# Optimization experiments

Measured on AMD Instinct MI355X. Metric: run time of the kernel, lower is better.

Reference implementation:

```python
import jax, jax.numpy as jnp
import numpy as np

N_NODES = 50000
N_EDGES = 800000
IN_FEAT = 256
OUT_FEAT = 256
NUM_RELS = 64
NUM_BASES = 8


def setup_inputs() -> dict:
    key = jax.random.key(0)
    ks = jax.random.split(key, 9)
    x = jax.random.normal(ks[0], (N_NODES, IN_FEAT), dtype=jnp.float32)
    src = jax.random.randint(ks[1], (N_EDGES,), 0, N_NODES, dtype=jnp.int32)
    dst = jax.random.randint(ks[2], (N_EDGES,), 0, N_NODES, dtype=jnp.int32)
    etypes = jax.random.randint(ks[3], (N_EDGES,), 0, NUM_RELS, dtype=jnp.int32)
    norm = jax.random.uniform(ks[4], (N_EDGES, 1), dtype=jnp.float32)
    # glorot-style params
    s_w = (6.0 / (IN_FEAT + OUT_FEAT)) ** 0.5
    weight = jax.random.uniform(ks[5], (NUM_BASES, IN_FEAT, OUT_FEAT), jnp.float32, -s_w, s_w)
    s_c = (6.0 / (NUM_RELS + NUM_BASES)) ** 0.5
    w_comp = jax.random.uniform(ks[6], (NUM_RELS, NUM_BASES), jnp.float32, -s_c, s_c)
    h_bias = jnp.zeros((OUT_FEAT,), jnp.float32)
    loop_weight = jax.random.uniform(ks[7], (IN_FEAT, OUT_FEAT), jnp.float32, -s_w, s_w)
    return {"x": x, "src": src, "dst": dst, "etypes": etypes, "norm": norm,
            "weight": weight, "w_comp": w_comp, "h_bias": h_bias,
            "loop_weight": loop_weight}


def reference(x, src, dst, etypes, norm, weight, w_comp, h_bias, loop_weight):
    # Basis regularizer with num_bases < num_rels:
    #   W_r = sum_b w_comp[r, b] * V_b
    # Per-edge message: msg_e = (x[src_e] @ W_{etype_e}) * norm_e,
    # aggregated by sum onto destination nodes. Since the map is linear,
    # we aggregate per basis first, then apply V_b (8 dense GEMMs).
    n_nodes = x.shape[0]
    coef = w_comp[etypes]                      # [E, B] per-edge basis coeffs
    xs = x[src] * norm                         # [E, D] normalized source feats
    out = jnp.zeros((n_nodes, weight.shape[2]), x.dtype)
    for b in range(weight.shape[0]):           # small fixed loop over bases
        agg = jax.ops.segment_sum(xs * coef[:, b:b + 1], dst,
                                  num_segments=n_nodes)   # [N, D]
        out = out + agg @ weight[b]            # [N, O]
    out = out + h_bias + x @ loop_weight       # bias + self-loop
    return jax.nn.relu(out)
```

## Files before the change

kernel.cpp:

```cpp
#include <hip/hip_runtime.h>
#include <hip/hip_bf16.h>
#include <stdint.h>

#define N_NODES 50000
#define N_EDGES 800000
#define IN_FEAT 256
#define OUT_FEAT 256
#define NUM_RELS 64
#define NUM_BASES 8
#define KTOT 2304
#define KAGG 2048
#define MP 50176
#define NT 36
#define SCAN_BLKS 196

typedef __attribute__((ext_vector_type(8))) __bf16 bf16x8;
typedef __attribute__((ext_vector_type(4))) __bf16 bf16x4;
typedef __attribute__((ext_vector_type(4))) float f32x4;
typedef __attribute__((ext_vector_type(2))) float f32x2;

static __device__ __forceinline__ void gload_lds16(const void* g, void* l) {
  auto gp = (const __attribute__((address_space(1))) void*)(uintptr_t)g;
  auto lp = (__attribute__((address_space(3))) void*)(uint32_t)(uintptr_t)l;
  __builtin_amdgcn_global_load_lds(gp, lp, 16, 0, 0);
}

__global__ void k_prex(const float* __restrict__ x, __bf16* __restrict__ xb) {
  int i = blockIdx.x * 256 + threadIdx.x;
  const float4* xp = (const float4*)x;
  float4 u = xp[i * 2], v = xp[i * 2 + 1];
  bf16x8 o;
  o[0] = (__bf16)u.x; o[1] = (__bf16)u.y; o[2] = (__bf16)u.z; o[3] = (__bf16)u.w;
  o[4] = (__bf16)v.x; o[5] = (__bf16)v.y; o[6] = (__bf16)v.z; o[7] = (__bf16)v.w;
  *(bf16x8*)(xb + (size_t)i * 8) = o;
}

__global__ void k_count(const int* __restrict__ dst, int* __restrict__ deg) {
  int e = blockIdx.x * 256 + threadIdx.x;
  atomicAdd(&deg[dst[e]], 1);
}

__global__ void k_scan1(const int* __restrict__ deg, int* __restrict__ offs,
                        int* __restrict__ bsum) {
  __shared__ int s[256];
  int t = threadIdx.x;
  int i = blockIdx.x * 256 + t;
  int v = (i < N_NODES) ? deg[i] : 0;
  s[t] = v;
  __syncthreads();
  for (int d = 1; d < 256; d <<= 1) {
    int y = (t >= d) ? s[t - d] : 0;
    __syncthreads();
    s[t] += y;
    __syncthreads();
  }
  if (i < N_NODES) offs[i] = s[t] - v;
  if (t == 255) bsum[blockIdx.x] = s[255];
}

__global__ void k_scan3(int* __restrict__ offs, const int* __restrict__ bsum,
                        int* __restrict__ fill) {
  __shared__ int s[256];
  int t = threadIdx.x;
  s[t] = (t < SCAN_BLKS && t < blockIdx.x) ? bsum[t] : 0;
  __syncthreads();
  for (int d = 128; d; d >>= 1) {
    if (t < d) s[t] += s[t + d];
    __syncthreads();
  }
  int base = s[0];
  int i = blockIdx.x * 256 + t;
  if (i < N_NODES) {
    int o = offs[i] + base;
    offs[i] = o;
    fill[i] = o;
  }
}

__global__ void k_scatter(const int* __restrict__ dst, const int* __restrict__ srcv,
                          const int* __restrict__ ety, const float* __restrict__ norm,
                          int* __restrict__ fill, uint2* __restrict__ erec) {
  int e = blockIdx.x * 256 + threadIdx.x;
  int pos = atomicAdd(&fill[dst[e]], 1);
  erec[pos] = make_uint2((unsigned)srcv[e] | ((unsigned)ety[e] << 16),
                         __float_as_uint(norm[e]));
}

#define AGG_BODY(RX, RY, XV)                                                  \
  do {                                                                        \
    int et_ = (RX) >> 16;                                                     \
    float nm_ = __uint_as_float(RY);                                          \
    f32x2 v0_ = {__uint_as_float((XV).x << 16) * nm_,                         \
                 __uint_as_float((XV).x & 0xffff0000u) * nm_};                 \
    f32x2 v1_ = {__uint_as_float((XV).y << 16) * nm_,                         \
                 __uint_as_float((XV).y & 0xffff0000u) * nm_};                 \
    f32x4 cl_ = *(const f32x4*)&wc[et_ * 8];                                  \
    f32x4 ch_ = *(const f32x4*)&wc[et_ * 8 + 4];                              \
    _Pragma("unroll") for (int b = 0; b < 4; ++b) {                           \
      acc[b][0] += v0_ * cl_[b];                                              \
      acc[b][1] += v1_ * cl_[b];                                              \
      acc[b + 4][0] += v0_ * ch_[b];                                          \
      acc[b + 4][1] += v1_ * ch_[b];                                          \
    }                                                                         \
  } while (0)

__global__ __launch_bounds__(256) void k_agg(
    const __bf16* __restrict__ xb, const float* __restrict__ w_comp,
    const int* __restrict__ offs, const int* __restrict__ fin,
    const uint2* __restrict__ erec, __bf16* __restrict__ A) {
  __shared__ float wc[NUM_RELS * NUM_BASES];
  int t = threadIdx.x;
  wc[t] = w_comp[t];
  wc[t + 256] = w_comp[t + 256];
  __syncthreads();

  int wid = t >> 6, lane = t & 63;
  int node = blockIdx.x * 4 + wid;

  f32x2 acc[NUM_BASES][2];
#pragma unroll
  for (int b = 0; b < NUM_BASES; ++b) {
    acc[b][0] = f32x2{0.f, 0.f};
    acc[b][1] = f32x2{0.f, 0.f};
  }

  int i0 = offs[node];
  int cnt = fin[node] - i0;
  const uint2* rp = erec + i0;
  int lo4 = lane * 4;

  int i = 0;
  for (; i + 8 <= cnt; i += 8) {
    uint2 r[8];
#pragma unroll
    for (int j = 0; j < 8; ++j) r[j] = rp[i + j];
    uint2 xv[8];
#pragma unroll
    for (int j = 0; j < 8; ++j)
      xv[j] = *(const uint2*)(xb + (size_t)(r[j].x & 0xffff) * IN_FEAT + lo4);
#pragma unroll
    for (int j = 0; j < 8; ++j) AGG_BODY(r[j].x, r[j].y, xv[j]);
  }
  for (; i + 4 <= cnt; i += 4) {
    uint2 r[4];
#pragma unroll
    for (int j = 0; j < 4; ++j) r[j] = rp[i + j];
    uint2 xv[4];
#pragma unroll
    for (int j = 0; j < 4; ++j)
      xv[j] = *(const uint2*)(xb + (size_t)(r[j].x & 0xffff) * IN_FEAT + lo4);
#pragma unroll
    for (int j = 0; j < 4; ++j) AGG_BODY(r[j].x, r[j].y, xv[j]);
  }
  for (; i < cnt; ++i) {
    uint2 r = rp[i];
    uint2 xv = *(const uint2*)(xb + (size_t)(r.x & 0xffff) * IN_FEAT + lo4);
    AGG_BODY(r.x, r.y, xv);
  }

  __bf16* Ar = A + (size_t)node * KAGG + lo4;
#pragma unroll
  for (int b = 0; b < NUM_BASES; ++b) {
    bf16x4 o;
    o[0] = (__bf16)acc[b][0][0];
    o[1] = (__bf16)acc[b][0][1];
    o[2] = (__bf16)acc[b][1][0];
    o[3] = (__bf16)acc[b][1][1];
    *(bf16x4*)(Ar + b * 256) = o;
  }
}

__global__ void k_prepwf(const float* __restrict__ weight, const float* __restrict__ loop_w,
                         __bf16* __restrict__ Wf) {
  int tid = blockIdx.x * 256 + threadIdx.x;
  int lane6 = tid & 63;
  int F = tid >> 6;
  int kt2 = F >> 4;
  int nf = F & 15;
  int o = nf * 16 + (lane6 & 15);
  int rbase = kt2 * 32 + (lane6 >> 4) * 8;
  bf16x8 v;
#pragma unroll
  for (int j = 0; j < 8; ++j) {
    int r = rbase + j;
    float f = (r < 2048) ? weight[(size_t)r * 256 + o]
                         : loop_w[(size_t)(r - 2048) * 256 + o];
    v[j] = (__bf16)f;
  }
  *(bf16x8*)(Wf + (size_t)tid * 8) = v;
}

__global__ __launch_bounds__(256, 2) void k_gemm(const __bf16* __restrict__ A,
                                                 const __bf16* __restrict__ xb,
                                                 const __bf16* __restrict__ Wf,
                                                 const float* __restrict__ bias,
                                                 float* __restrict__ out) {
  __shared__ __align__(16) __bf16 sA[3 * 64 * 64];

  int t = threadIdx.x;
  int wid = t >> 6, lane = t & 63;
  int tm = blockIdx.x;
  int rfw = __builtin_amdgcn_readfirstlane(wid);

  f32x4 acc[4][4];
#pragma unroll
  for (int m = 0; m < 4; ++m)
#pragma unroll
    for (int n = 0; n < 4; ++n) acc[m][n] = f32x4{0.f, 0.f, 0.f, 0.f};

  int frow = lane & 15;
  int g = lane >> 4;
  int f7 = frow & 7;
  int kb0 = ((g ^ f7) << 4);
  int kb1 = (((4 + g) ^ f7) << 4);

  int rh = t >> 3;
  int qoff = ((t & 7) ^ (rh & 7)) * 8;
  const __bf16* gA[2];
  const __bf16* gX[2];
#pragma unroll
  for (int it = 0; it < 2; ++it) {
    int row = it * 32 + rh;
    gA[it] = A + (size_t)(tm * 64 + row) * KAGG + qoff;
    gX[it] = xb + (size_t)(tm * 64 + row) * IN_FEAT + qoff;
  }
  const __bf16* wfb = Wf + (size_t)(wid * 4) * 512 + lane * 8;

  bf16x8 af[4][2], B0[4][2], B1[4][2];

#define VMWAIT(N) asm volatile("s_waitcnt vmcnt(" #N ")" ::: "memory")
#define BAR()                                       \
  do {                                              \
    asm volatile("" ::: "memory");                  \
    __builtin_amdgcn_s_barrier();                   \
    asm volatile("" ::: "memory");                  \
  } while (0)

#define STAGE(U, BUF)                                                         \
  do {                                                                        \
    char* d_ = (char*)sA + (BUF) * 8192;                                      \
    if ((U) < 32) {                                                           \
      int ko_ = (U) * 64;                                                     \
      gload_lds16(gA[0] + ko_, d_ + rfw * 1024);                              \
      gload_lds16(gA[1] + ko_, d_ + 4096 + rfw * 1024);                       \
    } else {                                                                  \
      int ko_ = ((U) - 32) * 64;                                              \
      gload_lds16(gX[0] + ko_, d_ + rfw * 1024);                              \
      gload_lds16(gX[1] + ko_, d_ + 4096 + rfw * 1024);                       \
    }                                                                         \
  } while (0)

#define LOADB(KT, DST)                                                        \
  do {                                                                        \
    _Pragma("unroll") for (int nf = 0; nf < 4; ++nf) {                        \
      DST[nf][0] = *(const bf16x8*)(wfb + (size_t)(((KT) * 2 + 0) * 16 + nf) * 512); \
      DST[nf][1] = *(const bf16x8*)(wfb + (size_t)(((KT) * 2 + 1) * 16 + nf) * 512); \
    }                                                                         \
  } while (0)

#define READ_A(BUF)                                                           \
  do {                                                                        \
    const char* b_ = (const char*)sA + (BUF) * 8192;                          \
    _Pragma("unroll") for (int mf = 0; mf < 4; ++mf) {                        \
      int r_ = mf * 16 + frow;                                                \
      af[mf][0] = *(const bf16x8*)(b_ + r_ * 128 + kb0);                      \
      af[mf][1] = *(const bf16x8*)(b_ + r_ * 128 + kb1);                      \
    }                                                                         \
  } while (0)

#define MFMA32(BS)                                                            \
  do {                                                                        \
    _Pragma("unroll") for (int mf = 0; mf < 4; ++mf)                          \
    _Pragma("unroll") for (int nf = 0; nf < 4; ++nf) {                        \
      acc[mf][nf] = __builtin_amdgcn_mfma_f32_16x16x32_bf16(                  \
          af[mf][0], BS[nf][0], acc[mf][nf], 0, 0, 0);                        \
      acc[mf][nf] = __builtin_amdgcn_mfma_f32_16x16x32_bf16(                  \
          af[mf][1], BS[nf][1], acc[mf][nf], 0, 0, 0);                        \
    }                                                                         \
  } while (0)

#define STEP(KT, BCUR, BNXT)                                                  \
  do {                                                                        \
    int cb_ = (KT) % 3;                                                       \
    int nb_ = ((KT) + 2) % 3;                                                 \
    int u2_ = ((KT) + 2 < NT) ? (KT) + 2 : NT - 1;                            \
    int un_ = ((KT) + 1 < NT) ? (KT) + 1 : NT - 1;                            \
    LOADB(un_, BNXT);               \
    STAGE(u2_, nb_);                \
    READ_A(cb_);                    \
    __builtin_amdgcn_s_setprio(1);                                            \
    MFMA32(BCUR);                   \
    __builtin_amdgcn_s_setprio(0);                                            \
    VMWAIT(10);                     \
    BAR();                          \
  } while (0)

  LOADB(0, B0);
  STAGE(0, 0);
  STAGE(1, 1);
  VMWAIT(2);
  BAR();

  for (int kt = 0; kt < NT; kt += 2) {
    STEP(kt, B0, B1);
    STEP(kt + 1, B1, B0);
  }
#undef STEP
#undef STAGE
#undef LOADB
#undef READ_A
#undef MFMA32
#undef VMWAIT
#undef BAR

  int r0 = (lane >> 4) * 4;
  int c0 = lane & 15;
#pragma unroll
  for (int m = 0; m < 4; ++m) {
    int rowb = tm * 64 + m * 16 + r0;
#pragma unroll
    for (int n = 0; n < 4; ++n) {
      int col = wid * 64 + n * 16 + c0;
      float bv = bias[col];
#pragma unroll
      for (int r = 0; r < 4; ++r) {
        int row = rowb + r;
        if (row < N_NODES) {
          float v = acc[m][n][r] + bv;
          out[(size_t)row * OUT_FEAT + col] = v > 0.f ? v : 0.f;
        }
      }
    }
  }
}

extern "C" void kernel_launch(void* const* d_in, const int* in_sizes, int n_in,
                              void* d_out, int out_size, void* d_ws, size_t ws_size,
                              hipStream_t stream) {
  const float* x      = (const float*)d_in[0];
  const int*   src    = (const int*)d_in[1];
  const int*   dst    = (const int*)d_in[2];
  const int*   ety    = (const int*)d_in[3];
  const float* norm   = (const float*)d_in[4];
  const float* weight = (const float*)d_in[5];
  const float* w_comp = (const float*)d_in[6];
  const float* h_bias = (const float*)d_in[7];
  const float* loop_w = (const float*)d_in[8];
  float* out = (float*)d_out;

  char* ws = (char*)d_ws;
  __bf16* A  = (__bf16*)ws;
  size_t off = (size_t)MP * KAGG * 2;
  __bf16* xb = (__bf16*)(ws + off);
  off += (size_t)MP * IN_FEAT * 2;
  __bf16* Wf = (__bf16*)(ws + off);
  off += (size_t)256 * KTOT * 2;
  uint2* erec = (uint2*)(ws + off);
  off += (size_t)N_EDGES * 8;
  int* deg   = (int*)(ws + off);
  int* offs  = deg + N_NODES;
  int* fill  = offs + N_NODES;
  int* bsum  = fill + N_NODES;

  hipMemsetAsync(deg, 0, N_NODES * sizeof(int), stream);
  k_prex<<<(N_NODES * IN_FEAT / 8) / 256, 256, 0, stream>>>(x, xb);
  k_count<<<N_EDGES / 256, 256, 0, stream>>>(dst, deg);
  k_scan1<<<SCAN_BLKS, 256, 0, stream>>>(deg, offs, bsum);
  k_scan3<<<SCAN_BLKS, 256, 0, stream>>>(offs, bsum, fill);
  k_scatter<<<N_EDGES / 256, 256, 0, stream>>>(dst, src, ety, norm, fill, erec);
  k_agg<<<N_NODES / 4, 256, 0, stream>>>(xb, w_comp, offs, fill, erec, A);
  k_prepwf<<<288, 256, 0, stream>>>(weight, loop_w, Wf);
  k_gemm<<<MP / 64, 256, 0, stream>>>(A, xb, Wf, h_bias, out);
}
```

Measured before the change: 301.1 us.

## Process two destination nodes per wavefront and read w_comp via scalar loads

The aggregation kernel now assigns two destination nodes to each wavefront and interleaves their edge loops in groups of four, so there are more independent gather loads in flight per wave. The per-relation coefficients are read straight from global memory using a wave-uniform (readfirstlane) index, which allows scalar loads in place of the LDS copy and its block barrier. Segment offsets are also made uniform. In exchange the doubled accumulator set raises register pressure, and unequal degrees between the two nodes leave tail imbalance.

```diff
diff --git a/kernel.cpp b/kernel.cpp
--- a/kernel.cpp
+++ b/kernel.cpp
@@ -86,87 +86,88 @@
                          __float_as_uint(norm[e]));
 }
 
-#define AGG_BODY(RX, RY, XV)                                                  \
-  do {                                                                        \
-    int et_ = (RX) >> 16;                                                     \
-    float nm_ = __uint_as_float(RY);                                          \
+#define AGGE(R, XV, ACC)                                                      \
+  do {                                                                        \
+    int et_ = __builtin_amdgcn_readfirstlane((int)((R).x >> 16));             \
+    float nm_ = __uint_as_float((R).y);                                       \
     f32x2 v0_ = {__uint_as_float((XV).x << 16) * nm_,                         \
                  __uint_as_float((XV).x & 0xffff0000u) * nm_};                 \
     f32x2 v1_ = {__uint_as_float((XV).y << 16) * nm_,                         \
                  __uint_as_float((XV).y & 0xffff0000u) * nm_};                 \
-    f32x4 cl_ = *(const f32x4*)&wc[et_ * 8];                                  \
-    f32x4 ch_ = *(const f32x4*)&wc[et_ * 8 + 4];                              \
+    f32x4 cl_ = *(const f32x4*)(w_comp + et_ * 8);                            \
+    f32x4 ch_ = *(const f32x4*)(w_comp + et_ * 8 + 4);                        \
     _Pragma("unroll") for (int b = 0; b < 4; ++b) {                           \
-      acc[b][0] += v0_ * cl_[b];                                              \
-      acc[b][1] += v1_ * cl_[b];                                              \
-      acc[b + 4][0] += v0_ * ch_[b];                                          \
-      acc[b + 4][1] += v1_ * ch_[b];                                          \
-    }                                                                         \
+      ACC[b][0] += v0_ * cl_[b];                                              \
+      ACC[b][1] += v1_ * cl_[b];                                              \
+      ACC[b + 4][0] += v0_ * ch_[b];                                          \
+      ACC[b + 4][1] += v1_ * ch_[b];                                          \
+    }                                                                         \
+  } while (0)
+
+#define EDGE4(RP, I, ACC)                                                     \
+  do {                                                                        \
+    uint2 r0_ = (RP)[(I) + 0], r1_ = (RP)[(I) + 1];                           \
+    uint2 r2_ = (RP)[(I) + 2], r3_ = (RP)[(I) + 3];                           \
+    uint2 x0_ = *(const uint2*)(xb + (size_t)(r0_.x & 0xffffu) * IN_FEAT + lo4);\
+    uint2 x1_ = *(const uint2*)(xb + (size_t)(r1_.x & 0xffffu) * IN_FEAT + lo4);\
+    uint2 x2_ = *(const uint2*)(xb + (size_t)(r2_.x & 0xffffu) * IN_FEAT + lo4);\
+    uint2 x3_ = *(const uint2*)(xb + (size_t)(r3_.x & 0xffffu) * IN_FEAT + lo4);\
+    AGGE(r0_, x0_, ACC); AGGE(r1_, x1_, ACC);                                 \
+    AGGE(r2_, x2_, ACC); AGGE(r3_, x3_, ACC);                                 \
+  } while (0)
+
+#define EDGE1(RP, I, ACC)                                                     \
+  do {                                                                        \
+    uint2 r_ = (RP)[(I)];                                                     \
+    uint2 x_ = *(const uint2*)(xb + (size_t)(r_.x & 0xffffu) * IN_FEAT + lo4);\
+    AGGE(r_, x_, ACC);                                                        \
   } while (0)
 
 __global__ __launch_bounds__(256) void k_agg(
     const __bf16* __restrict__ xb, const float* __restrict__ w_comp,
     const int* __restrict__ offs, const int* __restrict__ fin,
     const uint2* __restrict__ erec, __bf16* __restrict__ A) {
-  __shared__ float wc[NUM_RELS * NUM_BASES];
   int t = threadIdx.x;
-  wc[t] = w_comp[t];
-  wc[t + 256] = w_comp[t + 256];
-  __syncthreads();
-
   int wid = t >> 6, lane = t & 63;
-  int node = blockIdx.x * 4 + wid;
-
-  f32x2 acc[NUM_BASES][2];
+  int na = blockIdx.x * 8 + wid * 2;
+  int lo4 = lane * 4;
+
+  f32x2 acca[NUM_BASES][2], accb[NUM_BASES][2];
 #pragma unroll
   for (int b = 0; b < NUM_BASES; ++b) {
-    acc[b][0] = f32x2{0.f, 0.f};
-    acc[b][1] = f32x2{0.f, 0.f};
-  }
-
-  int i0 = offs[node];
-  int cnt = fin[node] - i0;
-  const uint2* rp = erec + i0;
-  int lo4 = lane * 4;
-
-  int i = 0;
-  for (; i + 8 <= cnt; i += 8) {
-    uint2 r[8];
-#pragma unroll
-    for (int j = 0; j < 8; ++j) r[j] = rp[i + j];
-    uint2 xv[8];
-#pragma unroll
-    for (int j = 0; j < 8; ++j)
-      xv[j] = *(const uint2*)(xb + (size_t)(r[j].x & 0xffff) * IN_FEAT + lo4);
-#pragma unroll
-    for (int j = 0; j < 8; ++j) AGG_BODY(r[j].x, r[j].y, xv[j]);
-  }
-  for (; i + 4 <= cnt; i += 4) {
-    uint2 r[4];
-#pragma unroll
-    for (int j = 0; j < 4; ++j) r[j] = rp[i + j];
-    uint2 xv[4];
-#pragma unroll
-    for (int j = 0; j < 4; ++j)
-      xv[j] = *(const uint2*)(xb + (size_t)(r[j].x & 0xffff) * IN_FEAT + lo4);
-#pragma unroll
-    for (int j = 0; j < 4; ++j) AGG_BODY(r[j].x, r[j].y, xv[j]);
-  }
-  for (; i < cnt; ++i) {
-    uint2 r = rp[i];
-    uint2 xv = *(const uint2*)(xb + (size_t)(r.x & 0xffff) * IN_FEAT + lo4);
-    AGG_BODY(r.x, r.y, xv);
-  }
-
-  __bf16* Ar = A + (size_t)node * KAGG + lo4;
+    acca[b][0] = f32x2{0.f, 0.f}; acca[b][1] = f32x2{0.f, 0.f};
+    accb[b][0] = f32x2{0.f, 0.f}; accb[b][1] = f32x2{0.f, 0.f};
+  }
+
+  int i0a = __builtin_amdgcn_readfirstlane(offs[na]);
+  int ca  = __builtin_amdgcn_readfirstlane(fin[na]) - i0a;
+  int i0b = __builtin_amdgcn_readfirstlane(offs[na + 1]);
+  int cb  = __builtin_amdgcn_readfirstlane(fin[na + 1]) - i0b;
+  const uint2* rpa = erec + i0a;
+  const uint2* rpb = erec + i0b;
+
+  int ia = 0, ib = 0;
+  int mm = (ca < cb ? ca : cb) & ~3;
+  for (; ia < mm; ia += 4, ib += 4) {
+    EDGE4(rpa, ia, acca);
+    EDGE4(rpb, ib, accb);
+  }
+  for (; ia + 4 <= ca; ia += 4) EDGE4(rpa, ia, acca);
+  for (; ib + 4 <= cb; ib += 4) EDGE4(rpb, ib, accb);
+  for (; ia < ca; ++ia) EDGE1(rpa, ia, acca);
+  for (; ib < cb; ++ib) EDGE1(rpb, ib, accb);
+
+  __bf16* Ara = A + (size_t)na * KAGG + lo4;
+  __bf16* Arb = A + (size_t)(na + 1) * KAGG + lo4;
 #pragma unroll
   for (int b = 0; b < NUM_BASES; ++b) {
-    bf16x4 o;
-    o[0] = (__bf16)acc[b][0][0];
-    o[1] = (__bf16)acc[b][0][1];
-    o[2] = (__bf16)acc[b][1][0];
-    o[3] = (__bf16)acc[b][1][1];
-    *(bf16x4*)(Ar + b * 256) = o;
+    bf16x4 oa, ob;
+    oa[0] = (__bf16)acca[b][0][0]; oa[1] = (__bf16)acca[b][0][1];
+    oa[2] = (__bf16)acca[b][1][0]; oa[3] = (__bf16)acca[b][1][1];
+    *(bf16x4*)(Ara + b * 256) = oa;
+    ob[0] = (__bf16)accb[b][0][0]; ob[1] = (__bf16)accb[b][0][1];
+    ob[2] = (__bf16)accb[b][1][0]; ob[3] = (__bf16)accb[b][1][1];
+    *(bf16x4*)(Arb + b * 256) = ob;
   }
 }
 
@@ -285,14 +286,14 @@
     int nb_ = ((KT) + 2) % 3;                                                 \
     int u2_ = ((KT) + 2 < NT) ? (KT) + 2 : NT - 1;                            \
     int un_ = ((KT) + 1 < NT) ? (KT) + 1 : NT - 1;                            \
-    LOADB(un_, BNXT);               \
-    STAGE(u2_, nb_);                \
-    READ_A(cb_);                    \
+    LOADB(un_, BNXT);                                                         \
+    STAGE(u2_, nb_);                                                          \
+    READ_A(cb_);                                                              \
     __builtin_amdgcn_s_setprio(1);                                            \
-    MFMA32(BCUR);                   \
+    MFMA32(BCUR);                                                             \
     __builtin_amdgcn_s_setprio(0);                                            \
-    VMWAIT(10);                     \
-    BAR();                          \
+    VMWAIT(10);                                                               \
+    BAR();                                                                    \
   } while (0)
 
   LOADB(0, B0);
@@ -368,7 +369,7 @@
   k_scan1<<<SCAN_BLKS, 256, 0, stream>>>(deg, offs, bsum);
   k_scan3<<<SCAN_BLKS, 256, 0, stream>>>(offs, bsum, fill);
   k_scatter<<<N_EDGES / 256, 256, 0, stream>>>(dst, src, ety, norm, fill, erec);
-  k_agg<<<N_NODES / 4, 256, 0, stream>>>(xb, w_comp, offs, fill, erec, A);
+  k_agg<<<N_NODES / 8, 256, 0, stream>>>(xb, w_comp, offs, fill, erec, A);
   k_prepwf<<<288, 256, 0, stream>>>(weight, loop_w, Wf);
   k_gemm<<<MP / 64, 256, 0, stream>>>(A, xb, Wf, h_bias, out);
 }
```

Result: no change. 299.9 us (-0.4%).
